# Optimization experiments

Measured on AMD Instinct MI355X. Metric: run time of the kernel, lower is better.

## Reference

```python
import jax, jax.numpy as jnp
import numpy as np

B, MODES, L = 512, 1000, 64


def setup_inputs() -> dict:
    key = jax.random.key(0)
    ks = jax.random.split(key, 10)
    inp = {
        "params": jax.random.normal(ks[0], (B, MODES, L), dtype=jnp.float32),
        "wfft0_re": jax.random.uniform(ks[1], (L, MODES), dtype=jnp.float32),
        "wfft0_im": jax.random.uniform(ks[2], (L, MODES), dtype=jnp.float32),
        "wfft1_re": jax.random.uniform(ks[3], (L, MODES), dtype=jnp.float32),
        "wfft1_im": jax.random.uniform(ks[4], (L, MODES), dtype=jnp.float32),
        "wfft2_re": jax.random.uniform(ks[5], (L, MODES), dtype=jnp.float32),
        "wfft2_im": jax.random.uniform(ks[6], (L, MODES), dtype=jnp.float32),
        "lin1_w": jax.random.normal(ks[7], (MODES, L * MODES), dtype=jnp.float32) * 0.01,
        "lin1_b": jnp.zeros((MODES,), dtype=jnp.float32),
        "lin2_w": jax.random.normal(ks[8], (L, MODES), dtype=jnp.float32) * 0.05,
        "lin2_b": jnp.zeros((L,), dtype=jnp.float32),
    }
    return inp


def _stft_block(x, wfft):
    # x: (B, MODES, L) real or complex; wfft: (L, MODES) complex
    fx = jnp.fft.fft(x, norm="forward")            # FFT over last (layer) axis, scaled 1/L
    # Faithful to torch.einsum('bfp,mn->bfm', ...): sums over BOTH p and n
    y = jnp.einsum("bfp,mn->bfm", fx, wfft)         # (B, MODES, L)
    y = jnp.fft.ifft(y, norm="forward")             # unnormalized inverse (norm='forward')
    return jnp.tanh(y).real                         # complex tanh, then real part


def reference(params, wfft0_re, wfft0_im, wfft1_re, wfft1_im, wfft2_re, wfft2_im,
              lin1_w, lin1_b, lin2_w, lin2_b):
    w0 = wfft0_re + 1j * wfft0_im
    w1 = wfft1_re + 1j * wfft1_im
    w2 = wfft2_re + 1j * wfft2_im
    x = _stft_block(params, w0)
    x = _stft_block(x, w1)
    x = _stft_block(x, w2)
    x = x.reshape(x.shape[0], -1)                   # (B, MODES*L), row-major like torch.flatten
    x = jnp.tanh(x @ lin1_w.T + lin1_b)             # (B, MODES)
    x = jax.nn.sigmoid(x @ lin2_w.T + lin2_b)       # (B, L)
    return x
```

## Files before the change

### kernel.cpp

```cpp
#include <hip/hip_runtime.h>
#include <math.h>

#define NB 512
#define MODES 1000
#define LL 64
#define PI_D 3.14159265358979323846

#define OFF_PART   0
#define OFF_SCAL   4096
#define OFF_T2RE   4224
#define OFF_T2IM   4736
#define OFF_GP     5248
#define OFF_CNT    5504
#define OFF_W2T    16384
#define OFF_S2     2621440
#define OFF_IRR    4718592
#define OFF_SG     13107200
#define OFF_EHI    19398656
#define OFF_ELO    21495808
#define OFF_SGNB   23592960
#define OFF_H      24641536

typedef short short8 __attribute__((ext_vector_type(8)));
typedef float f32x4 __attribute__((ext_vector_type(4)));

__device__ __forceinline__ double retanh_d(double a, double b) {
    if (fabs(a) > 20.0) return a > 0.0 ? 1.0 : -1.0;
    double e2 = exp(2.0 * a);
    double em2 = 1.0 / e2;
    return (e2 - em2) / (e2 + em2 + 2.0 * cos(2.0 * b));
}

__device__ __forceinline__ unsigned short f2bf(float x) {
    unsigned u = __float_as_uint(x);
    unsigned r = (u + 0x7FFFu + ((u >> 16) & 1u)) >> 16;
    return (unsigned short)r;
}

__global__ void k_misc(const float* __restrict__ w0r, const float* __restrict__ w0i,
                       const float* __restrict__ w1r, const float* __restrict__ w1i,
                       const float* __restrict__ w2r, const float* __restrict__ w2i,
                       const float* __restrict__ w2, char* ws) {
    int bid = blockIdx.x, t = threadIdx.x;
    if (bid < 192) {
        int k = bid >> 6, m = bid & 63;
        const float* wr = (k == 0) ? w0r : (k == 1) ? w1r : w2r;
        const float* wi = (k == 0) ? w0i : (k == 1) ? w1i : w2i;
        double sr = 0.0, si = 0.0;
        for (int c = t; c < MODES; c += 256) {
            sr += (double)wr[m * MODES + c];
            si += (double)wi[m * MODES + c];
        }
        __shared__ double lr[256], li[256];
        lr[t] = sr; li[t] = si; __syncthreads();
        for (int s = 128; s > 0; s >>= 1) {
            if (t < s) { lr[t] += lr[t + s]; li[t] += li[t + s]; }
            __syncthreads();
        }
        if (t == 0) {
            double2* p = (double2*)(ws + OFF_PART);
            p[k * 64 + m] = make_double2(lr[0], li[0]);
        }
    } else if (bid < 442) {
        int idx = (bid - 192) * 256 + t;
        int o = idx >> 6, j = idx & 63;
        ((float*)(ws + OFF_W2T))[idx] = w2[j * MODES + o];
    } else if (bid < 490) {
        int idx = (bid - 442) * 256 + t;
        ((unsigned*)(ws + OFF_EHI))[512000 + idx] = 0u;
    } else if (bid < 538) {
        int idx = (bid - 490) * 256 + t;
        ((unsigned*)(ws + OFF_ELO))[512000 + idx] = 0u;
    } else {
        int idx = (bid - 538) * 256 + t;
        if (idx < 6144) {
            int b = idx / 12, u = idx % 12;
            ((unsigned*)(ws + OFF_SGNB))[b * 512 + 500 + u] = 0u;
        }
    }
}

__global__ void k_prep(char* ws) {
    int t = threadIdx.x;
    int j = t & 63, q = t >> 6;
    double2* part = (double2*)(ws + OFF_PART);
    double* scal  = (double*)(ws + OFF_SCAL);
    double* t2re  = (double*)(ws + OFF_T2RE);
    double* t2im  = (double*)(ws + OFF_T2IM);
    float*  gp    = (float*)(ws + OFF_GP);
    __shared__ double a1[128], a2[128];
    __shared__ double sre[64], sim[64];
    __shared__ double tc[64], tsn[64];
    __shared__ double pr[4][64], pi_[4][64];
    if (t < 128) {
        double2 v = part[t];
        a1[t] = v.x; a2[t] = v.y;
    }
    if (t < 64) {
        double2 v = part[128 + t];
        sre[t] = v.x; sim[t] = v.y;
    }
    if (t >= 128 && t < 192) {
        int r = t - 128;
        double s, c;
        sincos((double)r * (PI_D / 32.0), &s, &c);
        tc[r] = c; tsn[r] = s;
    }
    __syncthreads();
    for (int s = 32; s > 0; s >>= 1) {
        if (t < 128 && (t & 63) < s) { a1[t] += a1[t + s]; a2[t] += a2[t + s]; }
        __syncthreads();
    }
    if (t < 2) { scal[2 * t] = a1[t * 64]; scal[2 * t + 1] = a2[t * 64]; }
    double tr = 0.0, ti = 0.0;
    for (int mm = q * 16; mm < q * 16 + 16; ++mm) {
        int r = (j * mm) & 63;
        double c = tc[r], s = tsn[r];
        tr += sre[mm] * c - sim[mm] * s;
        ti += sre[mm] * s + sim[mm] * c;
    }
    pr[q][j] = tr; pi_[q][j] = ti;
    __syncthreads();
    if (t < 64) {
        double trr = pr[0][t] + pr[1][t] + pr[2][t] + pr[3][t];
        double tii = pi_[0][t] + pi_[1][t] + pi_[2][t] + pi_[3][t];
        t2re[t] = trr; t2im[t] = tii;
        gp[t] = (float)retanh_d(trr, tii);
    }
    if (t == 0) *(int*)(ws + OFF_CNT) = 0;
}

__global__ void k_s(const float* __restrict__ params, char* ws) {
    int idx = blockIdx.x * 512 + threadIdx.x;
    const double* scal = (const double*)(ws + OFF_SCAL);
    double c0r = scal[0], c0i = scal[1], c1r = scal[2], c1i = scal[3];
    float p0 = params[(size_t)idx * 64];
    double s1 = retanh_d((double)p0 * c0r, (double)p0 * c0i);
    float s1f = (float)s1;
    double s2 = retanh_d((double)s1f * c1r, (double)s1f * c1i);
    float s2f = (float)s2;
    float sg; bool irr = false;
    if (s2f == 1.0f)       sg = 1.0f;
    else if (s2f == -1.0f) sg = -1.0f;
    else { sg = (s2f >= 0.0f) ? 1.0f : -1.0f; irr = true; }
    ((float*)(ws + OFF_SG))[idx] = sg;
    ((float*)(ws + OFF_S2))[idx] = s2f;
    int b = idx / 1000, f = idx - b * 1000;
    ((unsigned short*)(ws + OFF_SGNB))[(size_t)b * 1024 + f] =
        (sg > 0.0f) ? (unsigned short)0x3F80 : (unsigned short)0xBF80;
    if (irr) {
        int pos = atomicAdd((int*)(ws + OFF_CNT), 1);
        ((int*)(ws + OFF_IRR))[pos] = idx;
    }
}

__global__ void __launch_bounds__(512) k_E(const float* __restrict__ w1, char* ws) {
    int bid = blockIdx.x;
    int o = bid >> 2, x = bid & 2 | (bid & 1);
    int t = threadIdx.x;
    const float4* w4 = (const float4*)w1;
    const float4* gp4 = (const float4*)(ws + OFF_GP);
    float4 g = gp4[t & 15];
    unsigned short* ehi = (unsigned short*)(ws + OFF_EHI);
    unsigned short* elo = (unsigned short*)(ws + OFF_ELO);
    size_t rowbase = (size_t)o * 16000;
    int cbase = (bid & 3) * 4096 + t;
    float4 v[8];
#pragma unroll
    for (int k = 0; k < 8; ++k) {
        int gidx = cbase + k * 512;
        int cidx = (gidx < 15999) ? gidx : 15999;
        v[k] = w4[rowbase + cidx];
    }
#pragma unroll
    for (int k = 0; k < 8; ++k) {
        int gidx = cbase + k * 512;
        float a = v[k].x * g.x + v[k].y * g.y + v[k].z * g.z + v[k].w * g.w;
        a = (gidx < 16000) ? a : 0.0f;
        a += __shfl_xor(a, 1);
        a += __shfl_xor(a, 2);
        a += __shfl_xor(a, 4);
        a += __shfl_xor(a, 8);
        if ((t & 15) == 0) {
            int f = (bid & 3) * 256 + k * 32 + (t >> 4);
            unsigned short hi = f2bf(a);
            float hif = __uint_as_float((unsigned)hi << 16);
            unsigned short lo = f2bf(a - hif);
            ehi[(size_t)o * 1024 + f] = hi;
            elo[(size_t)o * 1024 + f] = lo;
        }
    }
}

__global__ void __launch_bounds__(128) k_gemm(char* ws) {
    const unsigned short* sgnb = (const unsigned short*)(ws + OFF_SGNB);
    const unsigned short* ehi  = (const unsigned short*)(ws + OFF_EHI);
    const unsigned short* elo  = (const unsigned short*)(ws + OFF_ELO);
    float* h = (float*)(ws + OFF_H);
    int strip = blockIdx.x;
    int btile = blockIdx.y;
    int t = threadIdx.x;
    int wave = t >> 6, l = t & 63;
    int rc = l & 15, grp = l >> 4;
    int b0 = btile * 16;
    int o0 = strip * 64 + wave * 32;
    f32x4 acc0 = {0.f, 0.f, 0.f, 0.f}, acc1 = {0.f, 0.f, 0.f, 0.f};
    const unsigned short* ap  = sgnb + (size_t)(b0 + rc) * 1024 + grp * 8;
    const unsigned short* bh0 = ehi + (size_t)(o0 + rc) * 1024 + grp * 8;
    const unsigned short* bl0 = elo + (size_t)(o0 + rc) * 1024 + grp * 8;
#pragma unroll 4
    for (int s = 0; s < 32; ++s) {
        short8 af  = *(const short8*)(ap + s * 32);
        short8 h0  = *(const short8*)(bh0 + s * 32);
        short8 l0  = *(const short8*)(bl0 + s * 32);
        short8 h1  = *(const short8*)(bh0 + 16 * 1024 + s * 32);
        short8 l1  = *(const short8*)(bl0 + 16 * 1024 + s * 32);
        acc0 = __builtin_amdgcn_mfma_f32_16x16x32_bf16(af, h0, acc0, 0, 0, 0);
        acc0 = __builtin_amdgcn_mfma_f32_16x16x32_bf16(af, l0, acc0, 0, 0, 0);
        acc1 = __builtin_amdgcn_mfma_f32_16x16x32_bf16(af, h1, acc1, 0, 0, 0);
        acc1 = __builtin_amdgcn_mfma_f32_16x16x32_bf16(af, l1, acc1, 0, 0, 0);
    }
#pragma unroll
    for (int r = 0; r < 4; ++r) {
        h[(size_t)(b0 + grp * 4 + r) * 1024 + o0 + rc]      = acc0[r];
        h[(size_t)(b0 + grp * 4 + r) * 1024 + o0 + 16 + rc] = acc1[r];
    }
}

__global__ void k_final(const float* __restrict__ w1, const float* __restrict__ b1,
                        const float* __restrict__ b2, float* __restrict__ out, char* ws) {
    int b = blockIdx.x, t = threadIdx.x;
    const float* hbuf = (const float*)(ws + OFF_H);
    __shared__ float h[MODES];
    __shared__ float part[4][64];
    __shared__ __align__(16) float cv[64];
    for (int o = t; o < MODES; o += 256)
        h[o] = hbuf[(size_t)b * 1024 + o] + b1[o];
    __syncthreads();
    int cnt = *(const int*)(ws + OFF_CNT);
    if (cnt > 0) {
        const int* irr     = (const int*)(ws + OFF_IRR);
        const float* s2a   = (const float*)(ws + OFF_S2);
        const float* sgn   = (const float*)(ws + OFF_SG);
        const double* t2re = (const double*)(ws + OFF_T2RE);
        const double* t2im = (const double*)(ws + OFF_T2IM);
        const float* gp    = (const float*)(ws + OFF_GP);
        for (int e = 0; e < cnt; ++e) {
            int idx = irr[e];
            int bb = idx / 1000;
            if (bb != b) continue;
            int f = idx - bb * 1000;
            float s2 = s2a[idx];
            float sg = sgn[idx];
            if (t < 64) {
                double g = retanh_d((double)s2 * t2re[t], (double)s2 * t2im[t]);
                cv[t] = (float)g - sg * gp[t];
            }
            __syncthreads();
            const float4* w4 = (const float4*)w1;
            const float4* c4 = (const float4*)cv;
            for (int o = t; o < MODES; o += 256) {
                size_t base = (size_t)o * 16000 + (size_t)f * 16;
                float a = 0.0f;
#pragma unroll
                for (int r = 0; r < 16; ++r) {
                    float4 w = w4[base + r];
                    float4 c = c4[r];
                    a += w.x * c.x + w.y * c.y + w.z * c.z + w.w * c.w;
                }
                h[o] += a;
            }
            __syncthreads();
        }
    }
    for (int o = t; o < MODES; o += 256) h[o] = tanhf(h[o]);
    __syncthreads();
    const float* w2t = (const float*)(ws + OFF_W2T);
    int j = t & 63, c = t >> 6;
    float acc = 0.0f;
    for (int o = c * 250; o < c * 250 + 250; ++o) acc += h[o] * w2t[o * 64 + j];
    part[c][j] = acc;
    __syncthreads();
    if (t < 64) {
        float s = part[0][t] + part[1][t] + part[2][t] + part[3][t] + b2[t];
        out[b * 64 + t] = 1.0f / (1.0f + expf(-s));
    }
}

extern "C" void kernel_launch(void* const* d_in, const int* in_sizes, int n_in,
                              void* d_out, int out_size, void* d_ws, size_t ws_size,
                              hipStream_t stream) {
    const float* params = (const float*)d_in[0];
    const float* w0r = (const float*)d_in[1];
    const float* w0i = (const float*)d_in[2];
    const float* w1r = (const float*)d_in[3];
    const float* w1i = (const float*)d_in[4];
    const float* w2r = (const float*)d_in[5];
    const float* w2i = (const float*)d_in[6];
    const float* lin1w = (const float*)d_in[7];
    const float* lin1b = (const float*)d_in[8];
    const float* lin2w = (const float*)d_in[9];
    const float* lin2b = (const float*)d_in[10];
    char* ws = (char*)d_ws;
    float* out = (float*)d_out;

    k_misc<<<562, 256, 0, stream>>>(w0r, w0i, w1r, w1i, w2r, w2i, lin2w, ws);
    k_prep<<<1, 256, 0, stream>>>(ws);
    k_s<<<1000, 512, 0, stream>>>(params, ws);
    k_E<<<4000, 512, 0, stream>>>(lin1w, ws);
    k_gemm<<<dim3(16, 32), 128, 0, stream>>>(ws);
    k_final<<<512, 256, 0, stream>>>(lin1w, lin1b, lin2b, out, ws);
}
```

Before: 110.7 us.

## Fuse prep, sign-scalar and E-projection kernels into one launch with redundant per-block prep

Merges the single-block k_prep, k_s and k_E kernels into one 5000-block kernel. Each block redundantly recomputes the small scalar reductions and the 64-entry gp vector in shared memory, so the two extra launches and their serialization points go away. The counter reset moves into k_misc. In exchange, every block pays a small double-precision prologue with several syncthreads, and the fused kernel's shared memory use and register pressure may lower occupancy for the bandwidth-bound E part.

```diff
diff --git a/kernel.cpp b/kernel.cpp
--- a/kernel.cpp
+++ b/kernel.cpp
@@ -3,7 +3,6 @@
 
 #define NB 512
 #define MODES 1000
-#define LL 64
 #define PI_D 3.14159265358979323846
 
 #define OFF_PART   0
@@ -42,6 +41,7 @@
                        const float* __restrict__ w2r, const float* __restrict__ w2i,
                        const float* __restrict__ w2, char* ws) {
     int bid = blockIdx.x, t = threadIdx.x;
+    if (bid == 0 && t == 0) *(int*)(ws + OFF_CNT) = 0;
     if (bid < 192) {
         int k = bid >> 6, m = bid & 63;
         const float* wr = (k == 0) ? w0r : (k == 1) ? w1r : w2r;
@@ -80,114 +80,124 @@
     }
 }
 
-__global__ void k_prep(char* ws) {
-    int t = threadIdx.x;
-    int j = t & 63, q = t >> 6;
-    double2* part = (double2*)(ws + OFF_PART);
-    double* scal  = (double*)(ws + OFF_SCAL);
-    double* t2re  = (double*)(ws + OFF_T2RE);
-    double* t2im  = (double*)(ws + OFF_T2IM);
-    float*  gp    = (float*)(ws + OFF_GP);
-    __shared__ double a1[128], a2[128];
-    __shared__ double sre[64], sim[64];
-    __shared__ double tc[64], tsn[64];
-    __shared__ double pr[4][64], pi_[4][64];
-    if (t < 128) {
-        double2 v = part[t];
-        a1[t] = v.x; a2[t] = v.y;
-    }
+__global__ void __launch_bounds__(512) k_sEb(const float* __restrict__ w1,
+                                             const float* __restrict__ params,
+                                             char* ws) {
+    __shared__ double a0r[64], a0i[64], a1r[64], a1i[64];
+    __shared__ double sre[64], sim[64], tc[64], tsn[64];
+    __shared__ double ppr[8][64], ppi[8][64];
+    __shared__ double scal_sh[4];
+    __shared__ double t2r_sh[64], t2i_sh[64];
+    __shared__ __align__(16) float gp_sh[64];
+    int bid = blockIdx.x, t = threadIdx.x;
+    const double2* part = (const double2*)(ws + OFF_PART);
     if (t < 64) {
-        double2 v = part[128 + t];
-        sre[t] = v.x; sim[t] = v.y;
-    }
-    if (t >= 128 && t < 192) {
-        int r = t - 128;
+        double2 v0 = part[t], v1 = part[64 + t], v2 = part[128 + t];
+        a0r[t] = v0.x; a0i[t] = v0.y;
+        a1r[t] = v1.x; a1i[t] = v1.y;
+        sre[t] = v2.x; sim[t] = v2.y;
+    } else if (t < 128) {
+        int r = t - 64;
         double s, c;
         sincos((double)r * (PI_D / 32.0), &s, &c);
         tc[r] = c; tsn[r] = s;
     }
     __syncthreads();
     for (int s = 32; s > 0; s >>= 1) {
-        if (t < 128 && (t & 63) < s) { a1[t] += a1[t + s]; a2[t] += a2[t + s]; }
+        if (t < s) {
+            a0r[t] += a0r[t + s]; a0i[t] += a0i[t + s];
+            a1r[t] += a1r[t + s]; a1i[t] += a1i[t + s];
+        }
         __syncthreads();
     }
-    if (t < 2) { scal[2 * t] = a1[t * 64]; scal[2 * t + 1] = a2[t * 64]; }
-    double tr = 0.0, ti = 0.0;
-    for (int mm = q * 16; mm < q * 16 + 16; ++mm) {
-        int r = (j * mm) & 63;
-        double c = tc[r], s = tsn[r];
-        tr += sre[mm] * c - sim[mm] * s;
-        ti += sre[mm] * s + sim[mm] * c;
-    }
-    pr[q][j] = tr; pi_[q][j] = ti;
+    if (t == 0) {
+        scal_sh[0] = a0r[0]; scal_sh[1] = a0i[0];
+        scal_sh[2] = a1r[0]; scal_sh[3] = a1i[0];
+    }
+    {
+        int j = t & 63, q = t >> 6;
+        double tr = 0.0, ti = 0.0;
+        for (int mm = q * 8; mm < q * 8 + 8; ++mm) {
+            int r = (j * mm) & 63;
+            double c = tc[r], s = tsn[r];
+            tr += sre[mm] * c - sim[mm] * s;
+            ti += sre[mm] * s + sim[mm] * c;
+        }
+        ppr[q][j] = tr; ppi[q][j] = ti;
+    }
     __syncthreads();
     if (t < 64) {
-        double trr = pr[0][t] + pr[1][t] + pr[2][t] + pr[3][t];
-        double tii = pi_[0][t] + pi_[1][t] + pi_[2][t] + pi_[3][t];
-        t2re[t] = trr; t2im[t] = tii;
-        gp[t] = (float)retanh_d(trr, tii);
-    }
-    if (t == 0) *(int*)(ws + OFF_CNT) = 0;
-}
-
-__global__ void k_s(const float* __restrict__ params, char* ws) {
-    int idx = blockIdx.x * 512 + threadIdx.x;
-    const double* scal = (const double*)(ws + OFF_SCAL);
-    double c0r = scal[0], c0i = scal[1], c1r = scal[2], c1i = scal[3];
-    float p0 = params[(size_t)idx * 64];
-    double s1 = retanh_d((double)p0 * c0r, (double)p0 * c0i);
-    float s1f = (float)s1;
-    double s2 = retanh_d((double)s1f * c1r, (double)s1f * c1i);
-    float s2f = (float)s2;
-    float sg; bool irr = false;
-    if (s2f == 1.0f)       sg = 1.0f;
-    else if (s2f == -1.0f) sg = -1.0f;
-    else { sg = (s2f >= 0.0f) ? 1.0f : -1.0f; irr = true; }
-    ((float*)(ws + OFF_SG))[idx] = sg;
-    ((float*)(ws + OFF_S2))[idx] = s2f;
-    int b = idx / 1000, f = idx - b * 1000;
-    ((unsigned short*)(ws + OFF_SGNB))[(size_t)b * 1024 + f] =
-        (sg > 0.0f) ? (unsigned short)0x3F80 : (unsigned short)0xBF80;
-    if (irr) {
-        int pos = atomicAdd((int*)(ws + OFF_CNT), 1);
-        ((int*)(ws + OFF_IRR))[pos] = idx;
-    }
-}
-
-__global__ void __launch_bounds__(512) k_E(const float* __restrict__ w1, char* ws) {
-    int bid = blockIdx.x;
-    int o = bid >> 2, x = bid & 2 | (bid & 1);
-    int t = threadIdx.x;
-    const float4* w4 = (const float4*)w1;
-    const float4* gp4 = (const float4*)(ws + OFF_GP);
-    float4 g = gp4[t & 15];
-    unsigned short* ehi = (unsigned short*)(ws + OFF_EHI);
-    unsigned short* elo = (unsigned short*)(ws + OFF_ELO);
-    size_t rowbase = (size_t)o * 16000;
-    int cbase = (bid & 3) * 4096 + t;
-    float4 v[8];
-#pragma unroll
-    for (int k = 0; k < 8; ++k) {
-        int gidx = cbase + k * 512;
-        int cidx = (gidx < 15999) ? gidx : 15999;
-        v[k] = w4[rowbase + cidx];
-    }
-#pragma unroll
-    for (int k = 0; k < 8; ++k) {
-        int gidx = cbase + k * 512;
-        float a = v[k].x * g.x + v[k].y * g.y + v[k].z * g.z + v[k].w * g.w;
-        a = (gidx < 16000) ? a : 0.0f;
-        a += __shfl_xor(a, 1);
-        a += __shfl_xor(a, 2);
-        a += __shfl_xor(a, 4);
-        a += __shfl_xor(a, 8);
-        if ((t & 15) == 0) {
-            int f = (bid & 3) * 256 + k * 32 + (t >> 4);
-            unsigned short hi = f2bf(a);
-            float hif = __uint_as_float((unsigned)hi << 16);
-            unsigned short lo = f2bf(a - hif);
-            ehi[(size_t)o * 1024 + f] = hi;
-            elo[(size_t)o * 1024 + f] = lo;
+        double tr = 0.0, ti = 0.0;
+#pragma unroll
+        for (int q = 0; q < 8; ++q) { tr += ppr[q][t]; ti += ppi[q][t]; }
+        t2r_sh[t] = tr; t2i_sh[t] = ti;
+        gp_sh[t] = (float)retanh_d(tr, ti);
+    }
+    __syncthreads();
+    if (bid == 0) {
+        if (t < 4) ((double*)(ws + OFF_SCAL))[t] = scal_sh[t];
+        if (t < 64) {
+            ((double*)(ws + OFF_T2RE))[t] = t2r_sh[t];
+            ((double*)(ws + OFF_T2IM))[t] = t2i_sh[t];
+            ((float*)(ws + OFF_GP))[t] = gp_sh[t];
+        }
+    }
+
+    if (bid < 1000) {
+        int idx = bid * 512 + t;
+        double c0r = scal_sh[0], c0i = scal_sh[1], c1r = scal_sh[2], c1i = scal_sh[3];
+        float p0 = params[(size_t)idx * 64];
+        double s1 = retanh_d((double)p0 * c0r, (double)p0 * c0i);
+        float s1f = (float)s1;
+        double s2 = retanh_d((double)s1f * c1r, (double)s1f * c1i);
+        float s2f = (float)s2;
+        float sg; bool irr = false;
+        if (s2f == 1.0f)       sg = 1.0f;
+        else if (s2f == -1.0f) sg = -1.0f;
+        else { sg = (s2f >= 0.0f) ? 1.0f : -1.0f; irr = true; }
+        ((float*)(ws + OFF_SG))[idx] = sg;
+        ((float*)(ws + OFF_S2))[idx] = s2f;
+        int b = idx / 1000, f = idx - b * 1000;
+        ((unsigned short*)(ws + OFF_SGNB))[(size_t)b * 1024 + f] =
+            (sg > 0.0f) ? (unsigned short)0x3F80 : (unsigned short)0xBF80;
+        if (irr) {
+            int pos = atomicAdd((int*)(ws + OFF_CNT), 1);
+            ((int*)(ws + OFF_IRR))[pos] = idx;
+        }
+    } else {
+        int eu = bid - 1000;
+        int o = eu >> 2, chunk = eu & 3;
+        const float4* w4 = (const float4*)w1;
+        const float4* gp4 = (const float4*)gp_sh;
+        float4 g = gp4[t & 15];
+        unsigned short* ehi = (unsigned short*)(ws + OFF_EHI);
+        unsigned short* elo = (unsigned short*)(ws + OFF_ELO);
+        size_t rowbase = (size_t)o * 16000;
+        int cbase = chunk * 4096 + t;
+        float4 v[8];
+#pragma unroll
+        for (int k = 0; k < 8; ++k) {
+            int gidx = cbase + k * 512;
+            int cidx = (gidx < 15999) ? gidx : 15999;
+            v[k] = w4[rowbase + cidx];
+        }
+#pragma unroll
+        for (int k = 0; k < 8; ++k) {
+            int gidx = cbase + k * 512;
+            float a = v[k].x * g.x + v[k].y * g.y + v[k].z * g.z + v[k].w * g.w;
+            a = (gidx < 16000) ? a : 0.0f;
+            a += __shfl_xor(a, 1);
+            a += __shfl_xor(a, 2);
+            a += __shfl_xor(a, 4);
+            a += __shfl_xor(a, 8);
+            if ((t & 15) == 0) {
+                int f = chunk * 256 + k * 32 + (t >> 4);
+                unsigned short hi = f2bf(a);
+                float hif = __uint_as_float((unsigned)hi << 16);
+                unsigned short lo = f2bf(a - hif);
+                ehi[(size_t)o * 1024 + f] = hi;
+                elo[(size_t)o * 1024 + f] = lo;
+            }
         }
     }
 }
@@ -305,9 +315,7 @@
     float* out = (float*)d_out;
 
     k_misc<<<562, 256, 0, stream>>>(w0r, w0i, w1r, w1i, w2r, w2i, lin2w, ws);
-    k_prep<<<1, 256, 0, stream>>>(ws);
-    k_s<<<1000, 512, 0, stream>>>(params, ws);
-    k_E<<<4000, 512, 0, stream>>>(lin1w, ws);
+    k_sEb<<<5000, 512, 0, stream>>>(lin1w, params, ws);
     k_gemm<<<dim3(16, 32), 128, 0, stream>>>(ws);
     k_final<<<512, 256, 0, stream>>>(lin1w, lin1b, lin2b, out, ws);
 }
```

Result: slower. 113.9 us (+3.0%).

## Split K dimension of the bf16 MFMA GEMM four ways, reduce partials in k_final

Applied to the files above, without the earlier changes.

The k_gemm launch gains a third grid dimension of 4. Each block now handles a quarter of the 1024-long reduction (8 steps instead of 32) and writes its partial results to a separate strided slice of the H buffer. k_final adds the four partial slices together with the bias when it loads h. The aim is four times as many GEMM blocks so the GPU's compute units are better filled, at the cost of extra partial-sum memory traffic and a larger workspace footprint. The k_E edits only rename a variable.

```diff
diff --git a/kernel.cpp b/kernel.cpp
--- a/kernel.cpp
+++ b/kernel.cpp
@@ -3,7 +3,6 @@
 
 #define NB 512
 #define MODES 1000
-#define LL 64
 #define PI_D 3.14159265358979323846
 
 #define OFF_PART   0
@@ -20,6 +19,7 @@
 #define OFF_ELO    21495808
 #define OFF_SGNB   23592960
 #define OFF_H      24641536
+#define HP_STRIDE  524288
 
 typedef short short8 __attribute__((ext_vector_type(8)));
 typedef float f32x4 __attribute__((ext_vector_type(4)));
@@ -156,7 +156,7 @@
 
 __global__ void __launch_bounds__(512) k_E(const float* __restrict__ w1, char* ws) {
     int bid = blockIdx.x;
-    int o = bid >> 2, x = bid & 2 | (bid & 1);
+    int o = bid >> 2, chunk = bid & 3;
     int t = threadIdx.x;
     const float4* w4 = (const float4*)w1;
     const float4* gp4 = (const float4*)(ws + OFF_GP);
@@ -164,7 +164,7 @@
     unsigned short* ehi = (unsigned short*)(ws + OFF_EHI);
     unsigned short* elo = (unsigned short*)(ws + OFF_ELO);
     size_t rowbase = (size_t)o * 16000;
-    int cbase = (bid & 3) * 4096 + t;
+    int cbase = chunk * 4096 + t;
     float4 v[8];
 #pragma unroll
     for (int k = 0; k < 8; ++k) {
@@ -182,7 +182,7 @@
         a += __shfl_xor(a, 4);
         a += __shfl_xor(a, 8);
         if ((t & 15) == 0) {
-            int f = (bid & 3) * 256 + k * 32 + (t >> 4);
+            int f = chunk * 256 + k * 32 + (t >> 4);
             unsigned short hi = f2bf(a);
             float hif = __uint_as_float((unsigned)hi << 16);
             unsigned short lo = f2bf(a - hif);
@@ -196,20 +196,21 @@
     const unsigned short* sgnb = (const unsigned short*)(ws + OFF_SGNB);
     const unsigned short* ehi  = (const unsigned short*)(ws + OFF_EHI);
     const unsigned short* elo  = (const unsigned short*)(ws + OFF_ELO);
-    float* h = (float*)(ws + OFF_H);
     int strip = blockIdx.x;
     int btile = blockIdx.y;
+    int z     = blockIdx.z;
+    float* hp = (float*)(ws + OFF_H) + (size_t)z * HP_STRIDE;
     int t = threadIdx.x;
     int wave = t >> 6, l = t & 63;
     int rc = l & 15, grp = l >> 4;
     int b0 = btile * 16;
     int o0 = strip * 64 + wave * 32;
     f32x4 acc0 = {0.f, 0.f, 0.f, 0.f}, acc1 = {0.f, 0.f, 0.f, 0.f};
-    const unsigned short* ap  = sgnb + (size_t)(b0 + rc) * 1024 + grp * 8;
-    const unsigned short* bh0 = ehi + (size_t)(o0 + rc) * 1024 + grp * 8;
-    const unsigned short* bl0 = elo + (size_t)(o0 + rc) * 1024 + grp * 8;
-#pragma unroll 4
-    for (int s = 0; s < 32; ++s) {
+    const unsigned short* ap  = sgnb + (size_t)(b0 + rc) * 1024 + z * 256 + grp * 8;
+    const unsigned short* bh0 = ehi + (size_t)(o0 + rc) * 1024 + z * 256 + grp * 8;
+    const unsigned short* bl0 = elo + (size_t)(o0 + rc) * 1024 + z * 256 + grp * 8;
+#pragma unroll
+    for (int s = 0; s < 8; ++s) {
         short8 af  = *(const short8*)(ap + s * 32);
         short8 h0  = *(const short8*)(bh0 + s * 32);
         short8 l0  = *(const short8*)(bl0 + s * 32);
@@ -222,20 +223,23 @@
     }
 #pragma unroll
     for (int r = 0; r < 4; ++r) {
-        h[(size_t)(b0 + grp * 4 + r) * 1024 + o0 + rc]      = acc0[r];
-        h[(size_t)(b0 + grp * 4 + r) * 1024 + o0 + 16 + rc] = acc1[r];
+        hp[(size_t)(b0 + grp * 4 + r) * 1024 + o0 + rc]      = acc0[r];
+        hp[(size_t)(b0 + grp * 4 + r) * 1024 + o0 + 16 + rc] = acc1[r];
     }
 }
 
 __global__ void k_final(const float* __restrict__ w1, const float* __restrict__ b1,
                         const float* __restrict__ b2, float* __restrict__ out, char* ws) {
     int b = blockIdx.x, t = threadIdx.x;
-    const float* hbuf = (const float*)(ws + OFF_H);
+    const float* hp = (const float*)(ws + OFF_H);
     __shared__ float h[MODES];
     __shared__ float part[4][64];
     __shared__ __align__(16) float cv[64];
-    for (int o = t; o < MODES; o += 256)
-        h[o] = hbuf[(size_t)b * 1024 + o] + b1[o];
+    for (int o = t; o < MODES; o += 256) {
+        size_t base = (size_t)b * 1024 + o;
+        h[o] = hp[base] + hp[base + HP_STRIDE] + hp[base + 2 * HP_STRIDE]
+             + hp[base + 3 * HP_STRIDE] + b1[o];
+    }
     __syncthreads();
     int cnt = *(const int*)(ws + OFF_CNT);
     if (cnt > 0) {
@@ -308,6 +312,6 @@
     k_prep<<<1, 256, 0, stream>>>(ws);
     k_s<<<1000, 512, 0, stream>>>(params, ws);
     k_E<<<4000, 512, 0, stream>>>(lin1w, ws);
-    k_gemm<<<dim3(16, 32), 128, 0, stream>>>(ws);
+    k_gemm<<<dim3(16, 32, 4), 128, 0, stream>>>(ws);
     k_final<<<512, 256, 0, stream>>>(lin1w, lin1b, lin2b, out, ws);
 }
```

Result: faster. 107.6 us (-2.8%).
